# Kernel tuning notes

Measured on AMD Instinct MI355X. Metric: run time of the kernel, lower is better.

The kernel has to match this reference:

```python
import jax, jax.numpy as jnp
import numpy as np

D_MODEL = 1024
N_HEADS = 16
HEAD_DIM = D_MODEL // N_HEADS
FOCUS_K = 64
LN_EPS = 1e-5


def setup_inputs() -> dict:
    key = jax.random.key(0)
    ks = jax.random.split(key, 16)
    B, T, N, d = 8, 2048, 32768, D_MODEL
    s = 0.02
    return {
        "h": jax.random.normal(ks[0], (B, T, d), jnp.float32),
        "memory": jax.random.normal(ks[1], (N, d), jnp.float32),
        "activations": jax.random.normal(ks[2], (B, N), jnp.float32),
        "ln_g": jnp.ones((d,), jnp.float32),
        "ln_b": jnp.zeros((d,), jnp.float32),
        "focus_w": jax.random.normal(ks[3], (d, d), jnp.float32) * s,
        "focus_b": jnp.zeros((d,), jnp.float32),
        "qw": jax.random.normal(ks[4], (d, d), jnp.float32) * s,
        "qb": jnp.zeros((d,), jnp.float32),
        "kw": jax.random.normal(ks[5], (d, d), jnp.float32) * s,
        "kb": jnp.zeros((d,), jnp.float32),
        "vw": jax.random.normal(ks[6], (d, d), jnp.float32) * s,
        "vb": jnp.zeros((d,), jnp.float32),
        "ow": jax.random.normal(ks[7], (d, d), jnp.float32) * s,
        "ob": jnp.zeros((d,), jnp.float32),
        "activation_weight": jnp.float32(1.0),
        "gate_logit": jnp.float32(0.0),
    }


def reference(h, memory, activations, ln_g, ln_b, focus_w, focus_b,
              qw, qb, kw, kb, vw, vb, ow, ob, activation_weight, gate_logit):
    B, T, d = h.shape
    N = memory.shape[0]
    K = min(FOCUS_K, N)
    H, Dh = N_HEADS, HEAD_DIM

    # LayerNorm
    mu = h.mean(-1, keepdims=True)
    var = jnp.var(h, axis=-1, keepdims=True)
    h_norm = (h - mu) * jax.lax.rsqrt(var + LN_EPS) * ln_g + ln_b

    # Focus query -> relevance over all N memory slots
    h_summary = h_norm.mean(axis=1)                    # (B, d)
    focus_query = h_summary @ focus_w + focus_b        # (B, d)
    relevance = focus_query @ memory.T                 # (B, N)
    selection = relevance + activation_weight * activations
    _, topk_idx = jax.lax.top_k(selection, K)          # (B, K)

    # Gather K memory vectors per batch
    topk_mem = memory[topk_idx]                        # (B, K, d)

    # Small-K cross-attention
    q = (h_norm @ qw + qb).reshape(B, T, H, Dh).transpose(0, 2, 1, 3)   # (B,H,T,Dh)
    k = (topk_mem @ kw + kb).reshape(B, K, H, Dh).transpose(0, 2, 1, 3)  # (B,H,K,Dh)
    v = (topk_mem @ vw + vb).reshape(B, K, H, Dh).transpose(0, 2, 1, 3)
    scores = jnp.einsum('bhtd,bhkd->bhtk', q, k) / (Dh ** 0.5)
    attn = jax.nn.softmax(scores, axis=-1)             # (B,H,T,K)
    out = jnp.einsum('bhtk,bhkd->bhtd', attn, v)
    out = out.transpose(0, 2, 1, 3).reshape(B, T, d)
    out = out @ ow + ob

    gate = jax.nn.sigmoid(gate_logit)
    h_updated = h + gate * out

    # Scatter mean attention back to full N
    mean_attn_topk = attn.mean(axis=(1, 2))            # (B, K)
    full_attn = jnp.zeros((B, N), h.dtype).at[jnp.arange(B)[:, None], topk_idx].set(mean_attn_topk)
    return h_updated, full_attn
```

## Files before the change

kernel.cpp:

```cpp
#include <hip/hip_runtime.h>

typedef unsigned short u16;
typedef unsigned int u32;
typedef __bf16 bf16x8 __attribute__((ext_vector_type(8)));
typedef float f32x4 __attribute__((ext_vector_type(4)));

#define DM 1024
#define B_ 8
#define T_ 2048
#define NN 32768
#define NH 16
#define DH 64
#define KF 64

__device__ __forceinline__ u16 f2bf(float f) {
  u32 x = __float_as_uint(f);
  x = (x + 0x7fffu + ((x >> 16) & 1u)) >> 16;
  return (u16)x;
}
__device__ __forceinline__ u32 mono(float f) {
  u32 x = __float_as_uint(f);
  return (x & 0x80000000u) ? ~x : (x | 0x80000000u);
}
__device__ __forceinline__ void async16(const void* g, void* s) {
  __builtin_amdgcn_global_load_lds((const __attribute__((address_space(1))) void*)g,
                                   (__attribute__((address_space(3))) void*)s, 16, 0, 0);
}

__global__ void k_zero(float* __restrict__ fullattn, float* __restrict__ colsum,
                       float* __restrict__ mattn) {
  int i = blockIdx.x * 256 + threadIdx.x;
  fullattn[i] = 0.f;
  if (i < B_ * DM) colsum[i] = 0.f;
  if (i < B_ * KF) mattn[i] = 0.f;
}

__global__ __launch_bounds__(256) void k_transpose(
    const float* __restrict__ w0, const float* __restrict__ w1,
    const float* __restrict__ w2, const float* __restrict__ w3,
    u16* __restrict__ o0, u16* __restrict__ o1, u16* __restrict__ o2, u16* __restrict__ o3) {
  __shared__ float t[32][33];
  const float* w = blockIdx.z == 0 ? w0 : blockIdx.z == 1 ? w1 : blockIdx.z == 2 ? w2 : w3;
  u16* o = blockIdx.z == 0 ? o0 : blockIdx.z == 1 ? o1 : blockIdx.z == 2 ? o2 : o3;
  int tx = threadIdx.x & 31, ty = threadIdx.x >> 5;
  int kb = blockIdx.y * 32, nb = blockIdx.x * 32;
#pragma unroll
  for (int j = 0; j < 32; j += 8) t[ty + j][tx] = w[(size_t)(kb + ty + j) * DM + nb + tx];
  __syncthreads();
#pragma unroll
  for (int j = 0; j < 32; j += 8) o[(size_t)(nb + ty + j) * DM + kb + tx] = f2bf(t[tx][ty + j]);
}

__global__ __launch_bounds__(256) void k_ln(const float* __restrict__ h, const float* __restrict__ g,
                                            const float* __restrict__ be, u16* __restrict__ hn,
                                            float* __restrict__ murstd) {
  int r = blockIdx.x, tid = threadIdx.x;
  float4 v = *(const float4*)(h + (size_t)r * DM + tid * 4);
  float s = v.x + v.y + v.z + v.w;
  float q = v.x * v.x + v.y * v.y + v.z * v.z + v.w * v.w;
#pragma unroll
  for (int off = 1; off < 64; off <<= 1) {
    s += __shfl_xor(s, off, 64);
    q += __shfl_xor(q, off, 64);
  }
  __shared__ float rs[4], rq[4];
  int w = tid >> 6;
  if ((tid & 63) == 0) { rs[w] = s; rq[w] = q; }
  __syncthreads();
  s = rs[0] + rs[1] + rs[2] + rs[3];
  q = rq[0] + rq[1] + rq[2] + rq[3];
  float mu = s * (1.f / 1024.f);
  float rstd = rsqrtf(q * (1.f / 1024.f) - mu * mu + 1e-5f);
  float4 gg = *(const float4*)(g + tid * 4);
  float4 bb = *(const float4*)(be + tid * 4);
  float n0 = (v.x - mu) * rstd * gg.x + bb.x;
  float n1 = (v.y - mu) * rstd * gg.y + bb.y;
  float n2 = (v.z - mu) * rstd * gg.z + bb.z;
  float n3 = (v.w - mu) * rstd * gg.w + bb.w;
  uint2 o;
  o.x = (u32)f2bf(n0) | ((u32)f2bf(n1) << 16);
  o.y = (u32)f2bf(n2) | ((u32)f2bf(n3) << 16);
  *(uint2*)(hn + (size_t)r * DM + tid * 4) = o;
  if (tid == 0) { murstd[r * 2] = mu; murstd[r * 2 + 1] = rstd; }
}

__global__ __launch_bounds__(256) void k_summary(const float* __restrict__ h,
                                                 const float* __restrict__ murstd,
                                                 float* __restrict__ colsum) {
  int col = blockIdx.x * 256 + threadIdx.x;
  int b = blockIdx.z;
  int tb = blockIdx.y * 128;
  float acc = 0.f;
  for (int t = 0; t < 128; ++t) {
    int r = b * T_ + tb + t;
    float mu = murstd[r * 2], rsd = murstd[r * 2 + 1];
    acc += (h[(size_t)r * DM + col] - mu) * rsd;
  }
  atomicAdd(&colsum[b * DM + col], acc);
}

__global__ __launch_bounds__(256) void k_focus(const float* __restrict__ colsum,
                                               const float* __restrict__ lng, const float* __restrict__ lnb,
                                               const float* __restrict__ fw, const float* __restrict__ fb,
                                               float* __restrict__ fq) {
  int gid = blockIdx.x * 256 + threadIdx.x;
  int b = gid >> 10, dout = gid & 1023;
  float acc = fb[dout];
  for (int i = 0; i < DM; ++i) {
    float hs = lng[i] * (colsum[b * DM + i] * (1.f / 2048.f)) + lnb[i];
    acc += hs * fw[(size_t)i * DM + dout];
  }
  fq[gid] = acc;
}

__global__ __launch_bounds__(256) void k_selection(const float* __restrict__ mem,
                                                   const float* __restrict__ fqg,
                                                   const float* __restrict__ act,
                                                   const float* __restrict__ awp,
                                                   float* __restrict__ sel) {
  __shared__ float fqs[8][1024];
  int tid = threadIdx.x;
#pragma unroll
  for (int i = 0; i < 8; ++i) {
    int e = i * 256 + tid;
    ((float4*)&fqs[0][0])[e] = ((const float4*)fqg)[e];
  }
  __syncthreads();
  float aw = awp[0];
  int l = tid & 63, w = tid >> 6;
  for (int n = blockIdx.x * 4 + w; n < NN; n += gridDim.x * 4) {
    const float* mrow = mem + (size_t)n * DM;
    float accb[8] = {0, 0, 0, 0, 0, 0, 0, 0};
#pragma unroll
    for (int c = 0; c < 4; ++c) {
      int d = c * 256 + l * 4;
      float4 mv = *(const float4*)(mrow + d);
#pragma unroll
      for (int b2 = 0; b2 < 8; ++b2) {
        float4 fv = *(const float4*)&fqs[b2][d];
        accb[b2] += mv.x * fv.x + mv.y * fv.y + mv.z * fv.z + mv.w * fv.w;
      }
    }
#pragma unroll
    for (int off = 1; off < 64; off <<= 1) {
#pragma unroll
      for (int b2 = 0; b2 < 8; ++b2) accb[b2] += __shfl_xor(accb[b2], off, 64);
    }
    if (l < 8) {
      float vsel = accb[0];
#pragma unroll
      for (int j = 1; j < 8; ++j) vsel = (l == j) ? accb[j] : vsel;
      sel[(size_t)l * NN + n] = vsel + aw * act[(size_t)l * NN + n];
    }
  }
}

#define CAND 1024
__global__ __launch_bounds__(1024) void k_topk(const float* __restrict__ sel, int* __restrict__ idx) {
  int b = blockIdx.x, tid = threadIdx.x;
  __shared__ u32 hist[256], hist2[256];
  __shared__ int scb, sA, ssb, sA2, nDef, nCand;
  __shared__ u32 cu[CAND];
  __shared__ int cn[CAND];
  __shared__ unsigned long long amax;
  if (tid < 256) { hist[tid] = 0; hist2[tid] = 0; }
  if (tid == 0) { nDef = 0; nCand = 0; }
  __syncthreads();
  const float* row = sel + (size_t)b * NN;
  for (int i = tid; i < NN; i += 1024) atomicAdd(&hist[mono(row[i]) >> 24], 1u);
  __syncthreads();
  if (tid < 256) {
    u32 s = 0;
    for (int j = tid + 1; j < 256; ++j) s += hist[j];
    if ((int)s < KF && (int)(s + hist[tid]) >= KF) { scb = tid; sA = (int)s; }
  }
  __syncthreads();
  int cb = scb;
  int R = KF - sA;
  for (int i = tid; i < NN; i += 1024) {
    u32 u = mono(row[i]);
    if ((int)(u >> 24) == cb) atomicAdd(&hist2[(u >> 16) & 255], 1u);
  }
  __syncthreads();
  if (tid < 256) {
    u32 s = 0;
    for (int j = tid + 1; j < 256; ++j) s += hist2[j];
    if ((int)s < R && (int)(s + hist2[tid]) >= R) { ssb = tid; sA2 = (int)s; }
  }
  __syncthreads();
  int R2 = R - sA2;
  u32 T16 = ((u32)cb << 8) | (u32)ssb;
  for (int i = tid; i < NN; i += 1024) {
    u32 u = mono(row[i]);
    u32 t = u >> 16;
    if (t > T16) {
      int p = atomicAdd(&nDef, 1);
      idx[b * KF + p] = i;
    } else if (t == T16) {
      int p = atomicAdd(&nCand, 1);
      if (p < CAND) { cu[p] = u; cn[p] = i; }
    }
  }
  __syncthreads();
  int base = nDef;
  int nc = nCand < CAND ? nCand : CAND;
  for (int r = 0; r < R2; ++r) {
    if (tid == 0) amax = 0;
    __syncthreads();
    unsigned long long loc = 0;
    for (int i = tid; i < nc; i += 1024) {
      unsigned long long key = ((unsigned long long)cu[i] << 32) | (u32)i;
      if (key > loc) loc = key;
    }
    if (loc) atomicMax(&amax, loc);
    __syncthreads();
    if (tid == 0) {
      int pos = (int)(amax & 0xffffffffu);
      idx[b * KF + base + r] = cn[pos];
      cu[pos] = 0;
    }
    __syncthreads();
  }
}

__global__ __launch_bounds__(256) void k_gather(const float* __restrict__ mem,
                                                const int* __restrict__ idx, u16* __restrict__ tm) {
  int rowi = blockIdx.x;
  int n = idx[rowi];
  float4 v = ((const float4*)(mem + (size_t)n * DM))[threadIdx.x];
  uint2 o;
  o.x = (u32)f2bf(v.x) | ((u32)f2bf(v.y) << 16);
  o.y = (u32)f2bf(v.z) | ((u32)f2bf(v.w) << 16);
  *(uint2*)(tm + (size_t)rowi * DM + threadIdx.x * 4) = o;
}

__global__ __launch_bounds__(256) void k_gemm(const u16* __restrict__ A, const u16* __restrict__ Bt,
                                              const float* __restrict__ bias, void* __restrict__ out,
                                              const float* __restrict__ hsrc, const float* __restrict__ gatep,
                                              int M, int N, int K, int mode) {
  __shared__ __align__(16) u16 As[128 * 32];
  __shared__ __align__(16) u16 Bs[128 * 32];
  int tid = threadIdx.x;
  int l = tid & 63, w = tid >> 6;
  int l15 = l & 15, quad = l >> 4;
  int wm = w >> 1, wn = w & 1;
  int m0 = blockIdx.x * 128, n0 = blockIdx.y * 128;
  int srow = w * 16 + (l >> 2);
  int koff = (l & 3) * 8;
  const u16* ga = A + (size_t)(m0 + srow) * K + koff;
  const u16* gb = Bt + (size_t)(n0 + srow) * K + koff;
  u16* lA0 = &As[(w * 16) * 32];
  u16* lA1 = &As[(64 + w * 16) * 32];
  u16* lB0 = &Bs[(w * 16) * 32];
  u16* lB1 = &Bs[(64 + w * 16) * 32];
  size_t rstride = (size_t)64 * K;
  f32x4 zero = {0.f, 0.f, 0.f, 0.f};
  f32x4 acc[4][4];
#pragma unroll
  for (int mt = 0; mt < 4; ++mt)
#pragma unroll
    for (int nt = 0; nt < 4; ++nt) acc[mt][nt] = zero;
  for (int kt = 0; kt < K; kt += 32) {
    __syncthreads();
    async16(ga + kt, lA0);
    async16(ga + rstride + kt, lA1);
    async16(gb + kt, lB0);
    async16(gb + rstride + kt, lB1);
    __syncthreads();
    bf16x8 af[4], bfr[4];
#pragma unroll
    for (int t = 0; t < 4; ++t) {
      af[t] = *(const bf16x8*)&As[(wm * 64 + t * 16 + l15) * 32 + quad * 8];
      bfr[t] = *(const bf16x8*)&Bs[(wn * 64 + t * 16 + l15) * 32 + quad * 8];
    }
#pragma unroll
    for (int mt = 0; mt < 4; ++mt)
#pragma unroll
      for (int nt = 0; nt < 4; ++nt)
        acc[mt][nt] = __builtin_amdgcn_mfma_f32_16x16x32_bf16(af[mt], bfr[nt], acc[mt][nt], 0, 0, 0);
  }
  float gv = 0.f;
  if (mode == 1) gv = 1.f / (1.f + __expf(-gatep[0]));
#pragma unroll
  for (int mt = 0; mt < 4; ++mt) {
#pragma unroll
    for (int nt = 0; nt < 4; ++nt) {
      int col = n0 + wn * 64 + nt * 16 + l15;
      float bv = bias[col];
#pragma unroll
      for (int reg = 0; reg < 4; ++reg) {
        int rrow = m0 + wm * 64 + mt * 16 + quad * 4 + reg;
        float v = acc[mt][nt][reg] + bv;
        if (mode == 0) {
          ((u16*)out)[(size_t)rrow * N + col] = f2bf(v);
        } else if (mode == 1) {
          size_t o = (size_t)rrow * N + col;
          ((float*)out)[o] = hsrc[o] + gv * v;
        } else {
          int bb = rrow >> 6, ks = rrow & 63, hh = col >> 6, dh = col & 63;
          size_t o;
          if (mode == 2) o = ((((size_t)bb * NH + hh) * KF + ks) * DH + dh);
          else o = ((((size_t)bb * NH + hh) * DH + dh) * KF + ks);
          ((u16*)out)[o] = f2bf(v);
        }
      }
    }
  }
}

__global__ __launch_bounds__(256) void k_attn(const u16* __restrict__ q, const u16* __restrict__ kk,
                                              const u16* __restrict__ vt, u16* __restrict__ o,
                                              float* __restrict__ mattn) {
  __shared__ u16 Qs[128][72];
  __shared__ u16 Ps[128][72];
  __shared__ u16 Ks[64][72];
  __shared__ u16 Vs[64][72];
  int tid = threadIdx.x;
  int t0 = blockIdx.x * 128, hh = blockIdx.y, b = blockIdx.z;
  {
    int row = tid >> 1, seg = tid & 1;
    const uint4* src = (const uint4*)(q + ((size_t)(b * T_ + t0 + row)) * DM + hh * DH + seg * 32);
#pragma unroll
    for (int j = 0; j < 4; ++j) *(uint4*)&Qs[row][seg * 32 + j * 8] = src[j];
  }
  {
    int row = tid >> 2, seg = tid & 3;
    size_t base = (((size_t)b * NH + hh) * 64 + row) * 64 + seg * 16;
    const uint4* sk = (const uint4*)(kk + base);
    const uint4* sv = (const uint4*)(vt + base);
    *(uint4*)&Ks[row][seg * 16] = sk[0];
    *(uint4*)&Ks[row][seg * 16 + 8] = sk[1];
    *(uint4*)&Vs[row][seg * 16] = sv[0];
    *(uint4*)&Vs[row][seg * 16 + 8] = sv[1];
  }
  __syncthreads();
  int l = tid & 63, w = tid >> 6;
  int l15 = l & 15, quad = l >> 4;
  f32x4 zero = {0.f, 0.f, 0.f, 0.f};
  f32x4 sacc[2][4];
#pragma unroll
  for (int mt = 0; mt < 2; ++mt)
#pragma unroll
    for (int nt = 0; nt < 4; ++nt) sacc[mt][nt] = zero;
#pragma unroll
  for (int step = 0; step < 2; ++step) {
    bf16x8 aq0 = *(const bf16x8*)&Qs[w * 32 + l15][step * 32 + quad * 8];
    bf16x8 aq1 = *(const bf16x8*)&Qs[w * 32 + 16 + l15][step * 32 + quad * 8];
#pragma unroll
    for (int nt = 0; nt < 4; ++nt) {
      bf16x8 bk = *(const bf16x8*)&Ks[nt * 16 + l15][step * 32 + quad * 8];
      sacc[0][nt] = __builtin_amdgcn_mfma_f32_16x16x32_bf16(aq0, bk, sacc[0][nt], 0, 0, 0);
      sacc[1][nt] = __builtin_amdgcn_mfma_f32_16x16x32_bf16(aq1, bk, sacc[1][nt], 0, 0, 0);
    }
  }
  float csum[4] = {0, 0, 0, 0};
#pragma unroll
  for (int mt = 0; mt < 2; ++mt) {
#pragma unroll
    for (int reg = 0; reg < 4; ++reg) {
      float s0 = sacc[mt][0][reg] * 0.125f;
      float s1 = sacc[mt][1][reg] * 0.125f;
      float s2 = sacc[mt][2][reg] * 0.125f;
      float s3 = sacc[mt][3][reg] * 0.125f;
      float mx = fmaxf(fmaxf(s0, s1), fmaxf(s2, s3));
#pragma unroll
      for (int off = 1; off < 16; off <<= 1) mx = fmaxf(mx, __shfl_xor(mx, off, 64));
      float p0 = __expf(s0 - mx), p1 = __expf(s1 - mx), p2 = __expf(s2 - mx), p3 = __expf(s3 - mx);
      float sum = p0 + p1 + p2 + p3;
#pragma unroll
      for (int off = 1; off < 16; off <<= 1) sum += __shfl_xor(sum, off, 64);
      float inv = 1.f / sum;
      p0 *= inv; p1 *= inv; p2 *= inv; p3 *= inv;
      int row = w * 32 + mt * 16 + quad * 4 + reg;
      Ps[row][0 * 16 + l15] = f2bf(p0);
      Ps[row][1 * 16 + l15] = f2bf(p1);
      Ps[row][2 * 16 + l15] = f2bf(p2);
      Ps[row][3 * 16 + l15] = f2bf(p3);
      csum[0] += p0; csum[1] += p1; csum[2] += p2; csum[3] += p3;
    }
  }
#pragma unroll
  for (int nt = 0; nt < 4; ++nt) {
    float v = csum[nt];
    v += __shfl_xor(v, 16, 64);
    v += __shfl_xor(v, 32, 64);
    if (quad == 0) atomicAdd(&mattn[b * KF + nt * 16 + l15], v);
  }
  __syncthreads();
  f32x4 oacc[2][4];
#pragma unroll
  for (int mt = 0; mt < 2; ++mt)
#pragma unroll
    for (int nt = 0; nt < 4; ++nt) oacc[mt][nt] = zero;
#pragma unroll
  for (int step = 0; step < 2; ++step) {
    bf16x8 ap0 = *(const bf16x8*)&Ps[w * 32 + l15][step * 32 + quad * 8];
    bf16x8 ap1 = *(const bf16x8*)&Ps[w * 32 + 16 + l15][step * 32 + quad * 8];
#pragma unroll
    for (int nt = 0; nt < 4; ++nt) {
      bf16x8 bv = *(const bf16x8*)&Vs[nt * 16 + l15][step * 32 + quad * 8];
      oacc[0][nt] = __builtin_amdgcn_mfma_f32_16x16x32_bf16(ap0, bv, oacc[0][nt], 0, 0, 0);
      oacc[1][nt] = __builtin_amdgcn_mfma_f32_16x16x32_bf16(ap1, bv, oacc[1][nt], 0, 0, 0);
    }
  }
#pragma unroll
  for (int mt = 0; mt < 2; ++mt)
#pragma unroll
    for (int nt = 0; nt < 4; ++nt)
#pragma unroll
      for (int reg = 0; reg < 4; ++reg) {
        int row = t0 + w * 32 + mt * 16 + quad * 4 + reg;
        int col = hh * DH + nt * 16 + l15;
        o[((size_t)(b * T_ + row)) * DM + col] = f2bf(oacc[mt][nt][reg]);
      }
}

__global__ void k_scatter(const float* __restrict__ mattn, const int* __restrict__ tidx,
                          float* __restrict__ out_attn) {
  int i = threadIdx.x;
  int b = i >> 6;
  out_attn[(size_t)b * NN + tidx[i]] = mattn[i] * (1.f / 32768.f);
}

extern "C" void kernel_launch(void* const* d_in, const int* in_sizes, int n_in,
                              void* d_out, int out_size, void* d_ws, size_t ws_size,
                              hipStream_t stream) {
  const float* h = (const float*)d_in[0];
  const float* mem = (const float*)d_in[1];
  const float* act = (const float*)d_in[2];
  const float* lng = (const float*)d_in[3];
  const float* lnb = (const float*)d_in[4];
  const float* fw = (const float*)d_in[5];
  const float* fb = (const float*)d_in[6];
  const float* qw = (const float*)d_in[7];
  const float* qb = (const float*)d_in[8];
  const float* kw = (const float*)d_in[9];
  const float* kb = (const float*)d_in[10];
  const float* vw = (const float*)d_in[11];
  const float* vb = (const float*)d_in[12];
  const float* ow = (const float*)d_in[13];
  const float* ob = (const float*)d_in[14];
  const float* awp = (const float*)d_in[15];
  const float* glp = (const float*)d_in[16];
  float* out_h = (float*)d_out;
  float* out_attn = out_h + (size_t)B_ * T_ * DM;

  char* p = (char*)d_ws;
  size_t off = 0;
  auto take = [&](size_t bytes) {
    void* r = p + off;
    off += (bytes + 255) & ~(size_t)255;
    return r;
  };
  u16* hnorm = (u16*)take((size_t)B_ * T_ * DM * 2);
  u16* q_ws = (u16*)take((size_t)B_ * T_ * DM * 2);
  u16* qwT = (u16*)take((size_t)DM * DM * 2);
  u16* kwT = (u16*)take((size_t)DM * DM * 2);
  u16* vwT = (u16*)take((size_t)DM * DM * 2);
  u16* owT = (u16*)take((size_t)DM * DM * 2);
  float* selw = (float*)take((size_t)B_ * NN * 4);
  u16* tmem = (u16*)take((size_t)B_ * KF * DM * 2);
  u16* k_ws = (u16*)take((size_t)B_ * NH * KF * DH * 2);
  u16* vT_ws = (u16*)take((size_t)B_ * NH * KF * DH * 2);
  float* murstd = (float*)take((size_t)B_ * T_ * 2 * 4);
  float* colsum = (float*)take((size_t)B_ * DM * 4);
  float* fq = (float*)take((size_t)B_ * DM * 4);
  float* mattn = (float*)take((size_t)B_ * KF * 4);
  int* tidx = (int*)take((size_t)B_ * KF * 4);
  u16* o_ws = hnorm;

  k_zero<<<1024, 256, 0, stream>>>(out_attn, colsum, mattn);
  k_transpose<<<dim3(32, 32, 4), 256, 0, stream>>>(qw, kw, vw, ow, qwT, kwT, vwT, owT);
  k_ln<<<B_ * T_, 256, 0, stream>>>(h, lng, lnb, hnorm, murstd);
  k_gemm<<<dim3(128, 8), 256, 0, stream>>>(hnorm, qwT, qb, q_ws, nullptr, nullptr, B_ * T_, DM, DM, 0);
  k_summary<<<dim3(4, 16, 8), 256, 0, stream>>>(h, murstd, colsum);
  k_focus<<<32, 256, 0, stream>>>(colsum, lng, lnb, fw, fb, fq);
  k_selection<<<2048, 256, 0, stream>>>(mem, fq, act, awp, selw);
  k_topk<<<8, 1024, 0, stream>>>(selw, tidx);
  k_gather<<<B_ * KF, 256, 0, stream>>>(mem, tidx, tmem);
  k_gemm<<<dim3(4, 8), 256, 0, stream>>>(tmem, kwT, kb, k_ws, nullptr, nullptr, B_ * KF, DM, DM, 2);
  k_gemm<<<dim3(4, 8), 256, 0, stream>>>(tmem, vwT, vb, vT_ws, nullptr, nullptr, B_ * KF, DM, DM, 3);
  k_attn<<<dim3(16, 16, 8), 256, 0, stream>>>(q_ws, k_ws, vT_ws, o_ws, mattn);
  k_gemm<<<dim3(128, 8), 256, 0, stream>>>(o_ws, owT, ob, out_h, h, glp, B_ * T_, DM, DM, 1);
  k_scatter<<<1, 512, 0, stream>>>(mattn, tidx, out_attn);
}
```

Before: 735.0 us.

## Double-buffer GEMM LDS with swizzle, merge K/V GEMMs, split-K focus projection

The GEMM kernel now double-buffers its LDS tiles so the next K-slice is loaded asynchronously while the current one feeds MFMA. It also applies an XOR-style rotation swizzle to the LDS layout to reduce bank conflicts on fragment reads. The K and V projections are fused into one launch through blockIdx.z. The focus projection is split across 8 K-slices with atomic accumulation to raise parallelism from 32 blocks, which requires zeroing fq first. Doubled LDS use may reduce occupancy, and the atomics make the fq sum order nondeterministic.

```diff
diff --git a/kernel.cpp b/kernel.cpp
--- a/kernel.cpp
+++ b/kernel.cpp
@@ -28,10 +28,10 @@
 }
 
 __global__ void k_zero(float* __restrict__ fullattn, float* __restrict__ colsum,
-                       float* __restrict__ mattn) {
+                       float* __restrict__ mattn, float* __restrict__ fq) {
   int i = blockIdx.x * 256 + threadIdx.x;
   fullattn[i] = 0.f;
-  if (i < B_ * DM) colsum[i] = 0.f;
+  if (i < B_ * DM) { colsum[i] = 0.f; fq[i] = 0.f; }
   if (i < B_ * KF) mattn[i] = 0.f;
 }
 
@@ -103,14 +103,16 @@
                                                const float* __restrict__ lng, const float* __restrict__ lnb,
                                                const float* __restrict__ fw, const float* __restrict__ fb,
                                                float* __restrict__ fq) {
-  int gid = blockIdx.x * 256 + threadIdx.x;
-  int b = gid >> 10, dout = gid & 1023;
-  float acc = fb[dout];
-  for (int i = 0; i < DM; ++i) {
+  int dout = blockIdx.x * 256 + threadIdx.x;
+  int slice = blockIdx.y;
+  int b = blockIdx.z;
+  float acc = (slice == 0) ? fb[dout] : 0.f;
+  int i0 = slice * 128;
+  for (int i = i0; i < i0 + 128; ++i) {
     float hs = lng[i] * (colsum[b * DM + i] * (1.f / 2048.f)) + lnb[i];
     acc += hs * fw[(size_t)i * DM + dout];
   }
-  fq[gid] = acc;
+  atomicAdd(&fq[b * DM + dout], acc);
 }
 
 __global__ __launch_bounds__(256) void k_selection(const float* __restrict__ mem,
@@ -234,44 +236,69 @@
   *(uint2*)(tm + (size_t)rowi * DM + threadIdx.x * 4) = o;
 }
 
-__global__ __launch_bounds__(256) void k_gemm(const u16* __restrict__ A, const u16* __restrict__ Bt,
-                                              const float* __restrict__ bias, void* __restrict__ out,
-                                              const float* __restrict__ hsrc, const float* __restrict__ gatep,
-                                              int M, int N, int K, int mode) {
-  __shared__ __align__(16) u16 As[128 * 32];
-  __shared__ __align__(16) u16 Bs[128 * 32];
+__global__ __launch_bounds__(256) void k_gemm(const u16* __restrict__ A,
+    const u16* __restrict__ Bt0, const float* __restrict__ bias0, void* __restrict__ out0, int mode0,
+    const u16* __restrict__ Bt1, const float* __restrict__ bias1, void* __restrict__ out1, int mode1,
+    const float* __restrict__ hsrc, const float* __restrict__ gatep, int M, int N, int K) {
+  __shared__ __align__(16) u16 As[2][128 * 32];
+  __shared__ __align__(16) u16 Bs[2][128 * 32];
+  const u16* Bt = blockIdx.z == 0 ? Bt0 : Bt1;
+  const float* bias = blockIdx.z == 0 ? bias0 : bias1;
+  void* out = blockIdx.z == 0 ? out0 : out1;
+  int mode = blockIdx.z == 0 ? mode0 : mode1;
   int tid = threadIdx.x;
   int l = tid & 63, w = tid >> 6;
   int l15 = l & 15, quad = l >> 4;
   int wm = w >> 1, wn = w & 1;
   int m0 = blockIdx.x * 128, n0 = blockIdx.y * 128;
-  int srow = w * 16 + (l >> 2);
-  int koff = (l & 3) * 8;
-  const u16* ga = A + (size_t)(m0 + srow) * K + koff;
-  const u16* gb = Bt + (size_t)(n0 + srow) * K + koff;
-  u16* lA0 = &As[(w * 16) * 32];
-  u16* lA1 = &As[(64 + w * 16) * 32];
-  u16* lB0 = &Bs[(w * 16) * 32];
-  u16* lB1 = &Bs[(64 + w * 16) * 32];
+  int r16 = l >> 2;
+  int rot = (r16 >> 1) & 3;
+  int q = ((l & 3) - rot) & 3;
+  int srow = w * 16 + r16;
+  const u16* ga = A + (size_t)(m0 + srow) * K + q * 8;
+  const u16* gb = Bt + (size_t)(n0 + srow) * K + q * 8;
   size_t rstride = (size_t)64 * K;
+  u16* lA0 = &As[0][(w * 16) * 32];
+  u16* lA1 = &As[0][(64 + w * 16) * 32];
+  u16* lB0 = &Bs[0][(w * 16) * 32];
+  u16* lB1 = &Bs[0][(64 + w * 16) * 32];
+  int aoff[4], boff[4];
+#pragma unroll
+  for (int t = 0; t < 4; ++t) {
+    int ra = wm * 64 + t * 16 + l15;
+    aoff[t] = ra * 32 + (((quad + ((ra >> 1) & 3)) & 3) << 3);
+    int rb = wn * 64 + t * 16 + l15;
+    boff[t] = rb * 32 + (((quad + ((rb >> 1) & 3)) & 3) << 3);
+  }
   f32x4 zero = {0.f, 0.f, 0.f, 0.f};
   f32x4 acc[4][4];
 #pragma unroll
   for (int mt = 0; mt < 4; ++mt)
 #pragma unroll
     for (int nt = 0; nt < 4; ++nt) acc[mt][nt] = zero;
-  for (int kt = 0; kt < K; kt += 32) {
+  const int iters = K >> 5;
+  async16(ga, lA0);
+  async16(ga + rstride, lA1);
+  async16(gb, lB0);
+  async16(gb + rstride, lB1);
+  for (int it = 0; it < iters; ++it) {
+    int cur = it & 1;
     __syncthreads();
-    async16(ga + kt, lA0);
-    async16(ga + rstride + kt, lA1);
-    async16(gb + kt, lB0);
-    async16(gb + rstride + kt, lB1);
-    __syncthreads();
+    if (it + 1 < iters) {
+      int kt = (it + 1) << 5;
+      int bo = (cur ^ 1) * 4096;
+      async16(ga + kt, lA0 + bo);
+      async16(ga + rstride + kt, lA1 + bo);
+      async16(gb + kt, lB0 + bo);
+      async16(gb + rstride + kt, lB1 + bo);
+    }
+    const u16* Ab = &As[cur][0];
+    const u16* Bb = &Bs[cur][0];
     bf16x8 af[4], bfr[4];
 #pragma unroll
     for (int t = 0; t < 4; ++t) {
-      af[t] = *(const bf16x8*)&As[(wm * 64 + t * 16 + l15) * 32 + quad * 8];
-      bfr[t] = *(const bf16x8*)&Bs[(wn * 64 + t * 16 + l15) * 32 + quad * 8];
+      af[t] = *(const bf16x8*)(Ab + aoff[t]);
+      bfr[t] = *(const bf16x8*)(Bb + boff[t]);
     }
 #pragma unroll
     for (int mt = 0; mt < 4; ++mt)
@@ -469,18 +496,23 @@
   int* tidx = (int*)take((size_t)B_ * KF * 4);
   u16* o_ws = hnorm;
 
-  k_zero<<<1024, 256, 0, stream>>>(out_attn, colsum, mattn);
+  k_zero<<<1024, 256, 0, stream>>>(out_attn, colsum, mattn, fq);
   k_transpose<<<dim3(32, 32, 4), 256, 0, stream>>>(qw, kw, vw, ow, qwT, kwT, vwT, owT);
   k_ln<<<B_ * T_, 256, 0, stream>>>(h, lng, lnb, hnorm, murstd);
-  k_gemm<<<dim3(128, 8), 256, 0, stream>>>(hnorm, qwT, qb, q_ws, nullptr, nullptr, B_ * T_, DM, DM, 0);
+  k_gemm<<<dim3(128, 8, 1), 256, 0, stream>>>(hnorm, qwT, qb, q_ws, 0,
+                                              nullptr, nullptr, nullptr, 0,
+                                              nullptr, nullptr, B_ * T_, DM, DM);
   k_summary<<<dim3(4, 16, 8), 256, 0, stream>>>(h, murstd, colsum);
-  k_focus<<<32, 256, 0, stream>>>(colsum, lng, lnb, fw, fb, fq);
+  k_focus<<<dim3(4, 8, 8), 256, 0, stream>>>(colsum, lng, lnb, fw, fb, fq);
   k_selection<<<2048, 256, 0, stream>>>(mem, fq, act, awp, selw);
   k_topk<<<8, 1024, 0, stream>>>(selw, tidx);
   k_gather<<<B_ * KF, 256, 0, stream>>>(mem, tidx, tmem);
-  k_gemm<<<dim3(4, 8), 256, 0, stream>>>(tmem, kwT, kb, k_ws, nullptr, nullptr, B_ * KF, DM, DM, 2);
-  k_gemm<<<dim3(4, 8), 256, 0, stream>>>(tmem, vwT, vb, vT_ws, nullptr, nullptr, B_ * KF, DM, DM, 3);
+  k_gemm<<<dim3(4, 8, 2), 256, 0, stream>>>(tmem, kwT, kb, k_ws, 2,
+                                            vwT, vb, vT_ws, 3,
+                                            nullptr, nullptr, B_ * KF, DM, DM);
   k_attn<<<dim3(16, 16, 8), 256, 0, stream>>>(q_ws, k_ws, vT_ws, o_ws, mattn);
-  k_gemm<<<dim3(128, 8), 256, 0, stream>>>(o_ws, owT, ob, out_h, h, glp, B_ * T_, DM, DM, 1);
+  k_gemm<<<dim3(128, 8, 1), 256, 0, stream>>>(o_ws, owT, ob, out_h, 1,
+                                              nullptr, nullptr, nullptr, 0,
+                                              h, glp, B_ * T_, DM, DM);
   k_scatter<<<1, 512, 0, stream>>>(mattn, tidx, out_attn);
 }
```

New measurement: 627.9 us. 1.17x faster.
